# Kernel tuning notes

Hardware: AMD Instinct MI355X
Metric: run time of the kernel (lower is better)

The kernel has to match this reference:

```python
import jax, jax.numpy as jnp
import numpy as np

TGT_NUM = 256  # init kwarg tgt_num


def setup_inputs() -> dict:
    key = jax.random.key(0)
    k1, k2 = jax.random.split(key)
    B, L, D = 64, 4096, 256
    video_feats = jax.random.normal(k1, (B, L, D), dtype=jnp.float32)
    video_masks = jax.random.randint(k2, (B, L), 0, 2).astype(bool)
    # guarantee at least one valid frame per video (torch code assumes src_num >= 1)
    video_masks = video_masks.at[:, 0].set(True)
    return {"video_feats": video_feats, "video_masks": video_masks}


def _aggregate_one(feats, mask, tgt_num):
    # feats: [L, D], mask: [L] bool
    L, D = feats.shape
    n = mask.sum()  # src_num (traced int)
    # compact valid frames to the front (equivalent of feats[mask]); OOB scatter
    # indices (== L) are dropped by default in jax scatters.
    cidx = jnp.cumsum(mask) - 1
    safe_idx = jnp.where(mask, cidx, L)
    comp = jnp.zeros_like(feats).at[safe_idx].set(feats)  # [L, D], valid rows first
    # bucket boundaries: round(k / tgt_num * n), clamped to n - 1  (round-half-even,
    # matching torch.round / jnp.round)
    k = jnp.arange(tgt_num + 1, dtype=jnp.float32)
    nf = n.astype(jnp.float32)
    idxs = jnp.minimum(jnp.round(k / tgt_num * nf), nf - 1.0).astype(jnp.int32)  # [T+1]
    s, e = idxs[:-1], idxs[1:]  # [T]
    j = jnp.arange(L, dtype=jnp.int32)[None, :]  # [1, L]
    in_range = (j >= s[:, None]) & (j < e[:, None])  # [T, L]
    denom = jnp.maximum(e - s, 1).astype(feats.dtype)  # avoid div-by-zero when s >= e
    mean_w = in_range.astype(feats.dtype) / denom[:, None]
    single_w = (j == s[:, None]).astype(feats.dtype)  # bucket is single row s when s >= e
    w = jnp.where((s < e)[:, None], mean_w, single_w)  # [T, L]
    return w @ comp  # [T, D]


def reference(video_feats, video_masks):
    agg = lambda f, m: _aggregate_one(f, m, TGT_NUM)
    return jax.vmap(agg)(video_feats, video_masks)  # [B, T, D]
```

## Files before the change

### kernel.cpp

```cpp
#include <hip/hip_runtime.h>
#include <stdint.h>

#define B_DIM 64
#define L_DIM 4096
#define D_DIM 256
#define TGT 256
#define BLK 512
#define ROWS_PER_BLOCK 16
#define NG (TGT / ROWS_PER_BLOCK)

__device__ __forceinline__ int idx_of(int k, float nf) {
    float x = rintf((float)k * (1.0f / 256.0f) * nf);
    x = fminf(x, nf - 1.0f);
    return (int)x;
}

__global__ __launch_bounds__(BLK)
void AggregateVideo_kernel(const uint8_t* __restrict__ mask_raw,
                           const float* __restrict__ feats,
                           float* __restrict__ out) {
    __shared__ unsigned short pos[L_DIM];
    __shared__ unsigned long long words[L_DIM / 64];
    __shared__ int pref[L_DIM / 64];
    __shared__ int flags[2];
    __shared__ int nsh;

    const int tid  = threadIdx.x;
    const int b    = blockIdx.y;
    const int g    = blockIdx.x;
    const int wv   = tid >> 6;
    const int lane = tid & 63;

    if (tid == 0) { flags[0] = 1; flags[1] = 1; }
    __syncthreads();
    {
        const uint32_t* mw = (const uint32_t*)mask_raw;
        bool bad_int = false, bad_f32 = false;
        #pragma unroll
        for (int i = 0; i < 2; ++i) {
            uint32_t w = mw[tid + BLK * i];
            if (w > 1u) bad_int = true;
            if (w != 0u && w != 0x3F800000u) bad_f32 = true;
        }
        if (bad_int) flags[0] = 0;
        if (bad_f32) flags[1] = 0;
    }
    __syncthreads();
    const int flag = flags[0] ? 1 : (flags[1] ? 2 : 0);

    {
        if (flag == 1) {
            const int32_t* m = (const int32_t*)mask_raw + (size_t)b * L_DIM;
            #pragma unroll
            for (int i = 0; i < L_DIM / BLK; ++i) {
                const int j = i * BLK + tid;
                unsigned long long bal = __ballot(m[j] != 0);
                if (lane == 0) words[j >> 6] = bal;
            }
        } else if (flag == 2) {
            const float* m = (const float*)mask_raw + (size_t)b * L_DIM;
            #pragma unroll
            for (int i = 0; i < L_DIM / BLK; ++i) {
                const int j = i * BLK + tid;
                unsigned long long bal = __ballot(m[j] != 0.0f);
                if (lane == 0) words[j >> 6] = bal;
            }
        } else {
            const uint8_t* m = mask_raw + (size_t)b * L_DIM;
            #pragma unroll
            for (int i = 0; i < L_DIM / BLK; ++i) {
                const int j = i * BLK + tid;
                unsigned long long bal = __ballot(m[j] != 0);
                if (lane == 0) words[j >> 6] = bal;
            }
        }
    }
    __syncthreads();

    if (tid < 64) {
        const unsigned long long wd = words[tid];
        const int c = __popcll(wd);
        int inc = c;
        #pragma unroll
        for (int off = 1; off < 64; off <<= 1) {
            int v = __shfl_up(inc, off);
            if (tid >= off) inc += v;
        }
        pref[tid] = inc - c;
        if (tid == 63) nsh = inc;
    }
    __syncthreads();

    {
        const int w      = tid >> 3;
        const int startb = (tid & 7) * 8;
        const unsigned long long wd = words[w];
        const unsigned long long below =
            startb ? (wd & ((1ull << startb) - 1ull)) : 0ull;
        int p = pref[w] + __popcll(below);
        const int base = w * 64 + startb;
        unsigned int byte = (unsigned int)((wd >> startb) & 0xFFull);
        while (byte) {
            const int bit = __ffs(byte) - 1;
            pos[p++] = (unsigned short)(base + bit);
            byte &= byte - 1;
        }
    }
    __syncthreads();

    const float nf = (float)nsh;
    const float* fb = feats + (size_t)b * L_DIM * D_DIM;

    #pragma unroll
    for (int rr = 0; rr < 2; ++rr) {
        const int t  = g * ROWS_PER_BLOCK + wv + rr * 8;
        const int s  = idx_of(t, nf);
        const int e  = idx_of(t + 1, nf);
        const int lo = s;
        const int hi = (e > s) ? e : (s + 1);
        const int cnt = hi - lo;
        const float inv = 1.0f / (float)cnt;

        const int myrow = (lane < cnt) ? (int)pos[lo + lane] : 0;

        float4 a0 = make_float4(0.f, 0.f, 0.f, 0.f);
        float4 a1 = make_float4(0.f, 0.f, 0.f, 0.f);
        float4 a2 = make_float4(0.f, 0.f, 0.f, 0.f);
        float4 a3 = make_float4(0.f, 0.f, 0.f, 0.f);
        int k = 0;
        for (; k + 4 <= cnt; k += 4) {
            const int r0 = __shfl(myrow, k);
            const int r1 = __shfl(myrow, k + 1);
            const int r2 = __shfl(myrow, k + 2);
            const int r3 = __shfl(myrow, k + 3);
            const float4 v0 = *((const float4*)(fb + (size_t)r0 * D_DIM) + lane);
            const float4 v1 = *((const float4*)(fb + (size_t)r1 * D_DIM) + lane);
            const float4 v2 = *((const float4*)(fb + (size_t)r2 * D_DIM) + lane);
            const float4 v3 = *((const float4*)(fb + (size_t)r3 * D_DIM) + lane);
            a0.x += v0.x; a0.y += v0.y; a0.z += v0.z; a0.w += v0.w;
            a1.x += v1.x; a1.y += v1.y; a1.z += v1.z; a1.w += v1.w;
            a2.x += v2.x; a2.y += v2.y; a2.z += v2.z; a2.w += v2.w;
            a3.x += v3.x; a3.y += v3.y; a3.z += v3.z; a3.w += v3.w;
        }
        for (; k < cnt; ++k) {
            const int r0 = __shfl(myrow, k);
            const float4 v0 = *((const float4*)(fb + (size_t)r0 * D_DIM) + lane);
            a0.x += v0.x; a0.y += v0.y; a0.z += v0.z; a0.w += v0.w;
        }
        a0.x += a1.x; a0.y += a1.y; a0.z += a1.z; a0.w += a1.w;
        a2.x += a3.x; a2.y += a3.y; a2.z += a3.z; a2.w += a3.w;
        a0.x += a2.x; a0.y += a2.y; a0.z += a2.z; a0.w += a2.w;
        a0.x *= inv; a0.y *= inv; a0.z *= inv; a0.w *= inv;
        *((float4*)(out + ((size_t)b * TGT + t) * D_DIM) + lane) = a0;
    }
}

extern "C" void kernel_launch(void* const* d_in, const int* in_sizes, int n_in,
                              void* d_out, int out_size, void* d_ws, size_t ws_size,
                              hipStream_t stream) {
    const float*   feats = (const float*)d_in[0];
    const uint8_t* masks = (const uint8_t*)d_in[1];
    float*         out   = (float*)d_out;
    (void)in_sizes; (void)n_in; (void)out_size; (void)d_ws; (void)ws_size;

    dim3 grid(NG, B_DIM);
    AggregateVideo_kernel<<<grid, BLK, 0, stream>>>(masks, feats, out);
}
```

Baseline: 31.71 us.

## Halve block size and interleave two output rows per wave with nontemporal loads

Shrinks blocks to 256 threads covering 8 output rows, which doubles the grid and the redundant per-block mask scan. Each wave now processes two output rows together in one loop, issuing their gathers interleaved instead of one row after another. Row indices come straight from shared memory rather than through wave shuffles. Loads and stores use nontemporal hints to avoid polluting cache. In exchange the four-way unrolled accumulation is gone, so fewer loads may be in flight per row, and the mask-compaction prologue now runs twice as many times in total.

```diff
diff --git a/kernel.cpp b/kernel.cpp
--- a/kernel.cpp
+++ b/kernel.cpp
@@ -5,9 +5,11 @@
 #define L_DIM 4096
 #define D_DIM 256
 #define TGT 256
-#define BLK 512
-#define ROWS_PER_BLOCK 16
+#define BLK 256
+#define ROWS_PER_BLOCK 8
 #define NG (TGT / ROWS_PER_BLOCK)
+
+typedef float f32x4 __attribute__((ext_vector_type(4)));
 
 __device__ __forceinline__ int idx_of(int k, float nf) {
     float x = rintf((float)k * (1.0f / 256.0f) * nf);
@@ -37,7 +39,7 @@
         const uint32_t* mw = (const uint32_t*)mask_raw;
         bool bad_int = false, bad_f32 = false;
         #pragma unroll
-        for (int i = 0; i < 2; ++i) {
+        for (int i = 0; i < 4; ++i) {
             uint32_t w = mw[tid + BLK * i];
             if (w > 1u) bad_int = true;
             if (w != 0u && w != 0x3F800000u) bad_f32 = true;
@@ -92,18 +94,18 @@
     __syncthreads();
 
     {
-        const int w      = tid >> 3;
-        const int startb = (tid & 7) * 8;
+        const int w      = tid >> 2;
+        const int startb = (tid & 3) * 16;
         const unsigned long long wd = words[w];
         const unsigned long long below =
             startb ? (wd & ((1ull << startb) - 1ull)) : 0ull;
         int p = pref[w] + __popcll(below);
         const int base = w * 64 + startb;
-        unsigned int byte = (unsigned int)((wd >> startb) & 0xFFull);
-        while (byte) {
-            const int bit = __ffs(byte) - 1;
+        unsigned int chunk = (unsigned int)((wd >> startb) & 0xFFFFull);
+        while (chunk) {
+            const int bit = __ffs(chunk) - 1;
             pos[p++] = (unsigned short)(base + bit);
-            byte &= byte - 1;
+            chunk &= chunk - 1;
         }
     }
     __syncthreads();
@@ -111,48 +113,45 @@
     const float nf = (float)nsh;
     const float* fb = feats + (size_t)b * L_DIM * D_DIM;
 
-    #pragma unroll
-    for (int rr = 0; rr < 2; ++rr) {
-        const int t  = g * ROWS_PER_BLOCK + wv + rr * 8;
-        const int s  = idx_of(t, nf);
-        const int e  = idx_of(t + 1, nf);
-        const int lo = s;
-        const int hi = (e > s) ? e : (s + 1);
-        const int cnt = hi - lo;
-        const float inv = 1.0f / (float)cnt;
+    const int t0  = g * ROWS_PER_BLOCK + wv;
+    const int t1  = t0 + 4;
 
-        const int myrow = (lane < cnt) ? (int)pos[lo + lane] : 0;
+    const int s0  = idx_of(t0, nf);
+    const int e0  = idx_of(t0 + 1, nf);
+    const int lo0 = s0;
+    const int hi0 = (e0 > s0) ? e0 : (s0 + 1);
+    const int c0  = hi0 - lo0;
+    const float inv0 = 1.0f / (float)c0;
 
-        float4 a0 = make_float4(0.f, 0.f, 0.f, 0.f);
-        float4 a1 = make_float4(0.f, 0.f, 0.f, 0.f);
-        float4 a2 = make_float4(0.f, 0.f, 0.f, 0.f);
-        float4 a3 = make_float4(0.f, 0.f, 0.f, 0.f);
-        int k = 0;
-        for (; k + 4 <= cnt; k += 4) {
-            const int r0 = __shfl(myrow, k);
-            const int r1 = __shfl(myrow, k + 1);
-            const int r2 = __shfl(myrow, k + 2);
-            const int r3 = __shfl(myrow, k + 3);
-            const float4 v0 = *((const float4*)(fb + (size_t)r0 * D_DIM) + lane);
-            const float4 v1 = *((const float4*)(fb + (size_t)r1 * D_DIM) + lane);
-            const float4 v2 = *((const float4*)(fb + (size_t)r2 * D_DIM) + lane);
-            const float4 v3 = *((const float4*)(fb + (size_t)r3 * D_DIM) + lane);
-            a0.x += v0.x; a0.y += v0.y; a0.z += v0.z; a0.w += v0.w;
-            a1.x += v1.x; a1.y += v1.y; a1.z += v1.z; a1.w += v1.w;
-            a2.x += v2.x; a2.y += v2.y; a2.z += v2.z; a2.w += v2.w;
-            a3.x += v3.x; a3.y += v3.y; a3.z += v3.z; a3.w += v3.w;
+    const int s1  = idx_of(t1, nf);
+    const int e1  = idx_of(t1 + 1, nf);
+    const int lo1 = s1;
+    const int hi1 = (e1 > s1) ? e1 : (s1 + 1);
+    const int c1  = hi1 - lo1;
+    const float inv1 = 1.0f / (float)c1;
+
+    const int cmax = (c0 > c1) ? c0 : c1;
+
+    f32x4 a0 = (f32x4)(0.f);
+    f32x4 a1 = (f32x4)(0.f);
+    for (int k = 0; k < cmax; ++k) {
+        if (k < c0) {
+            const int r = pos[lo0 + k];
+            const f32x4 v = __builtin_nontemporal_load(
+                (const f32x4*)(fb + (size_t)r * D_DIM) + lane);
+            a0 += v;
         }
-        for (; k < cnt; ++k) {
-            const int r0 = __shfl(myrow, k);
-            const float4 v0 = *((const float4*)(fb + (size_t)r0 * D_DIM) + lane);
-            a0.x += v0.x; a0.y += v0.y; a0.z += v0.z; a0.w += v0.w;
+        if (k < c1) {
+            const int r = pos[lo1 + k];
+            const f32x4 v = __builtin_nontemporal_load(
+                (const f32x4*)(fb + (size_t)r * D_DIM) + lane);
+            a1 += v;
         }
-        a0.x += a1.x; a0.y += a1.y; a0.z += a1.z; a0.w += a1.w;
-        a2.x += a3.x; a2.y += a3.y; a2.z += a3.z; a2.w += a3.w;
-        a0.x += a2.x; a0.y += a2.y; a0.z += a2.z; a0.w += a2.w;
-        a0.x *= inv; a0.y *= inv; a0.z *= inv; a0.w *= inv;
-        *((float4*)(out + ((size_t)b * TGT + t) * D_DIM) + lane) = a0;
     }
+    a0 *= inv0;
+    a1 *= inv1;
+    __builtin_nontemporal_store(a0, (f32x4*)(out + ((size_t)b * TGT + t0) * D_DIM) + lane);
+    __builtin_nontemporal_store(a1, (f32x4*)(out + ((size_t)b * TGT + t1) * D_DIM) + lane);
 }
 
 extern "C" void kernel_launch(void* const* d_in, const int* in_sizes, int n_in,
```

New measurement: 33.62 us. 6.0% more time.
